# Kernel tuning notes

Hardware: AMD Instinct MI355X
Metric: run time of the kernel (lower is better)

## Reference

```python
import jax, jax.numpy as jnp
import numpy as np

TEMPERATURE = 2.0 / 3.0
LIMIT_A = -0.1
LIMIT_B = 1.1

N_NODES = 50000
N_CLUSTERS = 64
N_RELATIONS = 8
N_EDGES = 1000000


def setup_inputs() -> dict:
    key = jax.random.key(0)
    ks = jax.random.split(key, 6)
    xavier = float(np.sqrt(6.0 / (N_CLUSTERS + N_CLUSTERS)))
    return {
        "assignments": jax.random.normal(ks[0], (N_NODES, N_CLUSTERS), jnp.float32),
        "inter_cluster_logits": jax.random.uniform(ks[1], (N_RELATIONS, N_CLUSTERS, N_CLUSTERS), jnp.float32, -xavier, xavier),
        "log_alpha": jnp.zeros((N_RELATIONS, N_CLUSTERS, N_CLUSTERS), jnp.float32),
        "absent_bias": jnp.zeros((N_RELATIONS,), jnp.float32),
        "edge_index": jax.random.randint(ks[2], (2, N_EDGES), 0, N_NODES, jnp.int32),
        "edge_type": jax.random.randint(ks[3], (N_EDGES,), 0, N_RELATIONS, jnp.int32),
        "neg_edge_index": jax.random.randint(ks[4], (2, N_EDGES), 0, N_NODES, jnp.int32),
        "neg_edge_type": jax.random.randint(ks[5], (N_EDGES,), 0, N_RELATIONS, jnp.int32),
    }


def _edge_logits(assignments, weights, absent_bias, edge_index, edge_type):
    # src, dst: [E, C] gathers (irregular access)
    src = assignments[edge_index[0]]
    dst = assignments[edge_index[1]]
    n_rel = weights.shape[0]
    # torch.bmm(W[et], dst[:, :, None]) == dst @ W[et].T ; compute per relation
    # (fixed small relation loop; avoids materializing [E, C, C]) then select.
    logits_all = jnp.stack(
        [jnp.sum(src * (dst @ weights[r].T), axis=-1) for r in range(n_rel)],
        axis=-1,
    )  # [E, R]
    logits = jnp.take_along_axis(logits_all, edge_type[:, None], axis=1)[:, 0]
    return logits + absent_bias[edge_type]


def reference(assignments, inter_cluster_logits, log_alpha, absent_bias,
              edge_index, edge_type, neg_edge_index, neg_edge_type):
    # Hard-concrete gate, eval mode: z = clamp(sigmoid(log_alpha)*(b-a)+a, 0, 1)
    gate = jnp.clip(jax.nn.sigmoid(log_alpha) * (LIMIT_B - LIMIT_A) + LIMIT_A, 0.0, 1.0)
    weights = jax.nn.sigmoid(inter_cluster_logits) * gate  # [R, C, C]

    pos_logits = _edge_logits(assignments, weights, absent_bias, edge_index, edge_type)
    neg_logits = _edge_logits(assignments, weights, absent_bias, neg_edge_index, neg_edge_type)

    # BCE-with-logits: target=1 -> softplus(-x); target=0 -> softplus(x)
    pos_loss = jnp.mean(jax.nn.softplus(-pos_logits))
    neg_loss = jnp.mean(jax.nn.softplus(neg_logits))
    return pos_loss + neg_loss
```

## Files before the change

kernel.cpp:

```cpp
#include <hip/hip_runtime.h>
#include <hip/hip_bf16.h>
#include <math.h>

#define E_EDGES 1000000
#define N_NODES 50000
#define N_C     64
#define N_REL   8
#define CHB     2048
#define CAP     384
#define NBLK    489
#define BT      512
#define SENT    0xFFFFFFFFu

typedef __attribute__((ext_vector_type(4))) float floatx4;
typedef __attribute__((ext_vector_type(2))) float floatx2;

static __device__ __forceinline__ unsigned pk4_fp8(float a, float b, float c, float d) {
    unsigned w = 0;
    w = __builtin_amdgcn_cvt_pk_fp8_f32(a, b, w, false);
    w = __builtin_amdgcn_cvt_pk_fp8_f32(c, d, w, true);
    return w;
}

static __device__ __forceinline__ long long pack64(unsigned lo, unsigned hi) {
    uint2 u; u.x = lo; u.y = hi;
    return __builtin_bit_cast(long long, u);
}

__global__ __launch_bounds__(256) void prep_kernel(
    const float* __restrict__ assign,
    const float* __restrict__ icl,
    const float* __restrict__ la,
    unsigned char* __restrict__ Wp8,
    unsigned char* __restrict__ AS8,
    float* __restrict__ out)
{
    int tid = blockIdx.x * blockDim.x + threadIdx.x;
    int nth = gridDim.x * blockDim.x;
    if (tid == 0) out[0] = 0.0f;

    for (int idx = tid; idx < N_REL * N_C * 16; idx += nth) {
        int row = idx >> 4, dq = idx & 15;
        int q = dq >> 2, c = (dq >> 1) & 1, jh = dq & 1;
        int k0 = (2 * c + jh) * 16 + 4 * q;
        float wv[4];
        #pragma unroll
        for (int b = 0; b < 4; ++b) {
            int srci = (row << 6) + k0 + b;
            float w = 1.0f / (1.0f + __expf(-icl[srci]));
            float g = 1.0f / (1.0f + __expf(-la[srci])) * 1.2f - 0.1f;
            g = fminf(fmaxf(g, 0.0f), 1.0f);
            wv[b] = w * g;
        }
        ((unsigned*)Wp8)[idx] = pk4_fp8(wv[0], wv[1], wv[2], wv[3]);
    }

    for (int n = tid; n < N_NODES; n += nth) {
        const float4* a4 = (const float4*)(assign + (size_t)n * N_C);
        unsigned w[16];
        #pragma unroll
        for (int i = 0; i < 16; ++i) {
            float4 v = a4[i];
            w[i] = pk4_fp8(v.x, v.y, v.z, v.w);
        }
        uint4* as = (uint4*)(AS8 + (size_t)n * N_C);
        #pragma unroll
        for (int q = 0; q < 4; ++q) {
            uint4 o;
            o.x = w[0 * 4 + q];
            o.y = w[1 * 4 + q];
            o.z = w[2 * 4 + q];
            o.w = w[3 * 4 + q];
            as[q] = o;
        }
    }
}

__global__ __launch_bounds__(BT, 8) void edge_kernel(
    const unsigned char* __restrict__ AS8,
    const unsigned char* __restrict__ Wp8,
    const float* __restrict__ absent_bias,
    const int* __restrict__ ei, const int* __restrict__ et,
    const int* __restrict__ nei, const int* __restrict__ net,
    float* __restrict__ out)
{
    __shared__ unsigned list[N_REL * CAP];
    __shared__ unsigned cnt[N_REL];
    __shared__ float red[8];
    if (threadIdx.x < N_REL) cnt[threadIdx.x] = 0u;
    __syncthreads();

    int blk = blockIdx.x;
    bool isneg = blk >= NBLK;
    int lb = isneg ? blk - NBLK : blk;
    const int* Es = isneg ? nei : ei;
    const int* Et = isneg ? net : et;
    float sign = isneg ? 1.0f : -1.0f;
    int base = lb * CHB;
    int elim = min(base + CHB, E_EDGES);

    for (int e = base + threadIdx.x; e < elim; e += BT) {
        int s = Es[e];
        int d = Es[E_EDGES + e];
        int r = Et[e];
        unsigned rank = atomicAdd(&cnt[r], 1u);
        if (rank < CAP) list[r * CAP + rank] = (unsigned)s | ((unsigned)d << 16);
    }
    __syncthreads();

    if (threadIdx.x < N_REL * 16) {
        int r = threadIdx.x >> 4;
        int i = threadIdx.x & 15;
        int n = min((int)cnt[r], CAP);
        int padded = ((n + 15) >> 4) << 4;
        int slot = n + i;
        if (slot < padded) list[r * CAP + slot] = SENT;
    }
    __syncthreads();

    int lane = threadIdx.x & 63;
    int wid  = threadIdx.x >> 6;
    int n16  = lane & 15;
    int quad = lane >> 4;
    float loss = 0.0f;

    int G0 = (min((int)cnt[0], CAP) + 15) >> 4;
    int G1 = (min((int)cnt[1], CAP) + 15) >> 4;
    int G2 = (min((int)cnt[2], CAP) + 15) >> 4;
    int G3 = (min((int)cnt[3], CAP) + 15) >> 4;
    int G4 = (min((int)cnt[4], CAP) + 15) >> 4;
    int G5 = (min((int)cnt[5], CAP) + 15) >> 4;
    int G6 = (min((int)cnt[6], CAP) + 15) >> 4;
    int G7 = (min((int)cnt[7], CAP) + 15) >> 4;
    int go1 = G0;
    int go2 = go1 + G1;
    int go3 = go2 + G2;
    int go4 = go3 + G3;
    int go5 = go4 + G4;
    int go6 = go5 + G5;
    int go7 = go6 + G6;
    int tg  = go7 + G7;

    #define LOCATE(ITEM, R, GOF)                                   \
        do {                                                       \
            R = 0; GOF = 0;                                        \
            if ((ITEM) >= go1) { R = 1; GOF = go1; }               \
            if ((ITEM) >= go2) { R = 2; GOF = go2; }               \
            if ((ITEM) >= go3) { R = 3; GOF = go3; }               \
            if ((ITEM) >= go4) { R = 4; GOF = go4; }               \
            if ((ITEM) >= go5) { R = 5; GOF = go5; }               \
            if ((ITEM) >= go6) { R = 6; GOF = go6; }               \
            if ((ITEM) >= go7) { R = 7; GOF = go7; }               \
        } while (0)

    #define FETCH(ITEM, R, V, SREG, DREG)                                    \
        do {                                                                 \
            int gof_;                                                        \
            LOCATE(ITEM, R, gof_);                                           \
            unsigned rec_ = list[R * CAP + ((ITEM) - gof_) * 16 + n16];      \
            V = rec_ != SENT;                                                \
            unsigned sm_ = V ? (rec_ & 0xFFFFu) : 0u;                        \
            unsigned dm_ = V ? (rec_ >> 16) : 0u;                            \
            SREG = *(const uint4*)(AS8 + ((size_t)sm_ << 6) + quad * 16);    \
            DREG = *(const uint4*)(AS8 + ((size_t)dm_ << 6) + quad * 16);    \
        } while (0)

    int start = (wid * tg) >> 3;
    int end   = ((wid + 1) * tg) >> 3;

    int rC = 0;
    bool vC = false;
    uint4 SC = {0, 0, 0, 0}, DC = {0, 0, 0, 0};
    uint4 wfm[4];
    float bias = 0.0f;

    if (start < end) {
        FETCH(start, rC, vC, SC, DC);
        #pragma unroll
        for (int mt = 0; mt < 4; ++mt)
            wfm[mt] = *(const uint4*)(Wp8 + ((rC * 64 + mt * 16 + n16) << 6) + quad * 16);
        bias = absent_bias[rC];
    }

    for (int it = start; it < end; ++it) {
        int rN = rC;
        bool vN = false;
        uint4 SN = {0, 0, 0, 0}, DN = {0, 0, 0, 0};
        if (it + 1 < end) {
            FETCH(it + 1, rN, vN, SN, DN);
        }

        long long bD0 = pack64(DC.x, DC.y);
        long long bD1 = pack64(DC.z, DC.w);
        floatx4 ac[4];
        #pragma unroll
        for (int mt = 0; mt < 4; ++mt) {
            floatx4 z = {0.0f, 0.0f, 0.0f, 0.0f};
            z = __builtin_amdgcn_mfma_f32_16x16x32_fp8_fp8(
                    pack64(wfm[mt].x, wfm[mt].y), bD0, z, 0, 0, 0);
            ac[mt] = __builtin_amdgcn_mfma_f32_16x16x32_fp8_fp8(
                    pack64(wfm[mt].z, wfm[mt].w), bD1, z, 0, 0, 0);
        }
        unsigned sw[4] = {SC.x, SC.y, SC.z, SC.w};
        float d0 = 0.0f, d1 = 0.0f;
        #pragma unroll
        for (int mt = 0; mt < 4; mt += 2) {
            floatx2 lo0 = __builtin_amdgcn_cvt_pk_f32_fp8((int)sw[mt], false);
            floatx2 hi0 = __builtin_amdgcn_cvt_pk_f32_fp8((int)sw[mt], true);
            floatx2 lo1 = __builtin_amdgcn_cvt_pk_f32_fp8((int)sw[mt + 1], false);
            floatx2 hi1 = __builtin_amdgcn_cvt_pk_f32_fp8((int)sw[mt + 1], true);
            d0 = fmaf(lo0.x, ac[mt][0], d0);
            d1 = fmaf(lo1.x, ac[mt + 1][0], d1);
            d0 = fmaf(lo0.y, ac[mt][1], d0);
            d1 = fmaf(lo1.y, ac[mt + 1][1], d1);
            d0 = fmaf(hi0.x, ac[mt][2], d0);
            d1 = fmaf(hi1.x, ac[mt + 1][2], d1);
            d0 = fmaf(hi0.y, ac[mt][3], d0);
            d1 = fmaf(hi1.y, ac[mt + 1][3], d1);
        }
        float dot = d0 + d1;
        dot += __shfl_xor(dot, 16);
        dot += __shfl_xor(dot, 32);
        if (quad == 0 && vC) {
            float x = sign * (dot + bias);
            loss += fmaxf(x, 0.0f) + __logf(1.0f + __expf(-fabsf(x)));
        }

        if (rN != rC) {
            #pragma unroll
            for (int mt = 0; mt < 4; ++mt)
                wfm[mt] = *(const uint4*)(Wp8 + ((rN * 64 + mt * 16 + n16) << 6) + quad * 16);
            bias = absent_bias[rN];
            rC = rN;
        }
        vC = vN; SC = SN; DC = DN;
    }

    loss += __shfl_xor(loss, 1);
    loss += __shfl_xor(loss, 2);
    loss += __shfl_xor(loss, 4);
    loss += __shfl_xor(loss, 8);
    loss += __shfl_xor(loss, 16);
    loss += __shfl_xor(loss, 32);
    if (lane == 0) red[wid] = loss;
    __syncthreads();
    if (threadIdx.x == 0) {
        float t = red[0] + red[1] + red[2] + red[3]
                + red[4] + red[5] + red[6] + red[7];
        atomicAdd(out, t * (1.0f / (float)E_EDGES));
    }
}

extern "C" void kernel_launch(void* const* d_in, const int* in_sizes, int n_in,
                              void* d_out, int out_size, void* d_ws, size_t ws_size,
                              hipStream_t stream) {
    const float* assign = (const float*)d_in[0];
    const float* icl    = (const float*)d_in[1];
    const float* la     = (const float*)d_in[2];
    const float* ab     = (const float*)d_in[3];
    const int*   ei     = (const int*)d_in[4];
    const int*   et     = (const int*)d_in[5];
    const int*   nei    = (const int*)d_in[6];
    const int*   net    = (const int*)d_in[7];
    float* out = (float*)d_out;

    char* basep = (char*)d_ws;
    unsigned char* Wp8 = (unsigned char*)basep;
    unsigned char* AS8 = (unsigned char*)(basep + 65536);

    prep_kernel<<<256, 256, 0, stream>>>(assign, icl, la, Wp8, AS8, out);
    edge_kernel<<<2 * NBLK, BT, 0, stream>>>(AS8, Wp8, ab, ei, et, nei, net, out);
}
```

Before: 133.7 us.

## Deepen gather prefetch to two items ahead and interleave MFMA with reduction

```diff
diff --git a/kernel.cpp b/kernel.cpp
--- a/kernel.cpp
+++ b/kernel.cpp
@@ -6,9 +6,9 @@
 #define N_NODES 50000
 #define N_C     64
 #define N_REL   8
-#define CHB     2048
+#define CHB     1954
 #define CAP     384
-#define NBLK    489
+#define NBLK    512
 #define BT      512
 #define SENT    0xFFFFFFFFu
 
@@ -168,72 +168,79 @@
     int start = (wid * tg) >> 3;
     int end   = ((wid + 1) * tg) >> 3;
 
-    int rC = 0;
-    bool vC = false;
-    uint4 SC = {0, 0, 0, 0}, DC = {0, 0, 0, 0};
+    int r0 = 0, r1 = 0;
+    bool v0 = false, v1 = false;
+    uint4 S0 = {0,0,0,0}, D0 = {0,0,0,0};
+    uint4 S1 = {0,0,0,0}, D1 = {0,0,0,0};
     uint4 wfm[4];
     float bias = 0.0f;
+    const floatx4 zero4 = {0.0f, 0.0f, 0.0f, 0.0f};
 
     if (start < end) {
-        FETCH(start, rC, vC, SC, DC);
+        FETCH(start, r0, v0, S0, D0);
         #pragma unroll
         for (int mt = 0; mt < 4; ++mt)
-            wfm[mt] = *(const uint4*)(Wp8 + ((rC * 64 + mt * 16 + n16) << 6) + quad * 16);
-        bias = absent_bias[rC];
+            wfm[mt] = *(const uint4*)(Wp8 + ((r0 * 64 + mt * 16 + n16) << 6) + quad * 16);
+        bias = absent_bias[r0];
+        r1 = r0;
+        if (start + 1 < end) {
+            FETCH(start + 1, r1, v1, S1, D1);
+        }
     }
 
     for (int it = start; it < end; ++it) {
-        int rN = rC;
-        bool vN = false;
-        uint4 SN = {0, 0, 0, 0}, DN = {0, 0, 0, 0};
-        if (it + 1 < end) {
-            FETCH(it + 1, rN, vN, SN, DN);
-        }
-
-        long long bD0 = pack64(DC.x, DC.y);
-        long long bD1 = pack64(DC.z, DC.w);
-        floatx4 ac[4];
-        #pragma unroll
-        for (int mt = 0; mt < 4; ++mt) {
-            floatx4 z = {0.0f, 0.0f, 0.0f, 0.0f};
-            z = __builtin_amdgcn_mfma_f32_16x16x32_fp8_fp8(
-                    pack64(wfm[mt].x, wfm[mt].y), bD0, z, 0, 0, 0);
-            ac[mt] = __builtin_amdgcn_mfma_f32_16x16x32_fp8_fp8(
-                    pack64(wfm[mt].z, wfm[mt].w), bD1, z, 0, 0, 0);
-        }
-        unsigned sw[4] = {SC.x, SC.y, SC.z, SC.w};
+        int r2 = r1;
+        bool v2 = false;
+        uint4 S2 = {0,0,0,0}, D2 = {0,0,0,0};
+        if (it + 2 < end) {
+            FETCH(it + 2, r2, v2, S2, D2);
+        }
+
+        long long bD0 = pack64(D0.x, D0.y);
+        long long bD1 = pack64(D0.z, D0.w);
+        unsigned sw[4] = {S0.x, S0.y, S0.z, S0.w};
         float d0 = 0.0f, d1 = 0.0f;
         #pragma unroll
-        for (int mt = 0; mt < 4; mt += 2) {
-            floatx2 lo0 = __builtin_amdgcn_cvt_pk_f32_fp8((int)sw[mt], false);
-            floatx2 hi0 = __builtin_amdgcn_cvt_pk_f32_fp8((int)sw[mt], true);
-            floatx2 lo1 = __builtin_amdgcn_cvt_pk_f32_fp8((int)sw[mt + 1], false);
-            floatx2 hi1 = __builtin_amdgcn_cvt_pk_f32_fp8((int)sw[mt + 1], true);
-            d0 = fmaf(lo0.x, ac[mt][0], d0);
-            d1 = fmaf(lo1.x, ac[mt + 1][0], d1);
-            d0 = fmaf(lo0.y, ac[mt][1], d0);
-            d1 = fmaf(lo1.y, ac[mt + 1][1], d1);
-            d0 = fmaf(hi0.x, ac[mt][2], d0);
-            d1 = fmaf(hi1.x, ac[mt + 1][2], d1);
-            d0 = fmaf(hi0.y, ac[mt][3], d0);
-            d1 = fmaf(hi1.y, ac[mt + 1][3], d1);
+        for (int gidx = 0; gidx < 2; ++gidx) {
+            const int ma = 2 * gidx, mb = 2 * gidx + 1;
+            floatx4 p0 = zero4, p1 = zero4;
+            p0 = __builtin_amdgcn_mfma_f32_16x16x32_fp8_fp8(
+                    pack64(wfm[ma].x, wfm[ma].y), bD0, p0, 0, 0, 0);
+            p1 = __builtin_amdgcn_mfma_f32_16x16x32_fp8_fp8(
+                    pack64(wfm[mb].x, wfm[mb].y), bD0, p1, 0, 0, 0);
+            p0 = __builtin_amdgcn_mfma_f32_16x16x32_fp8_fp8(
+                    pack64(wfm[ma].z, wfm[ma].w), bD1, p0, 0, 0, 0);
+            p1 = __builtin_amdgcn_mfma_f32_16x16x32_fp8_fp8(
+                    pack64(wfm[mb].z, wfm[mb].w), bD1, p1, 0, 0, 0);
+            floatx2 lo0 = __builtin_amdgcn_cvt_pk_f32_fp8((int)sw[ma], false);
+            floatx2 hi0 = __builtin_amdgcn_cvt_pk_f32_fp8((int)sw[ma], true);
+            floatx2 lo1 = __builtin_amdgcn_cvt_pk_f32_fp8((int)sw[mb], false);
+            floatx2 hi1 = __builtin_amdgcn_cvt_pk_f32_fp8((int)sw[mb], true);
+            d0 = fmaf(lo0.x, p0[0], d0);
+            d1 = fmaf(lo1.x, p1[0], d1);
+            d0 = fmaf(lo0.y, p0[1], d0);
+            d1 = fmaf(lo1.y, p1[1], d1);
+            d0 = fmaf(hi0.x, p0[2], d0);
+            d1 = fmaf(hi1.x, p1[2], d1);
+            d0 = fmaf(hi0.y, p0[3], d0);
+            d1 = fmaf(hi1.y, p1[3], d1);
         }
         float dot = d0 + d1;
         dot += __shfl_xor(dot, 16);
         dot += __shfl_xor(dot, 32);
-        if (quad == 0 && vC) {
+        if (quad == 0 && v0) {
             float x = sign * (dot + bias);
             loss += fmaxf(x, 0.0f) + __logf(1.0f + __expf(-fabsf(x)));
         }
 
-        if (rN != rC) {
+        if (r1 != r0) {
             #pragma unroll
             for (int mt = 0; mt < 4; ++mt)
-                wfm[mt] = *(const uint4*)(Wp8 + ((rN * 64 + mt * 16 + n16) << 6) + quad * 16);
-            bias = absent_bias[rN];
-            rC = rN;
-        }
-        vC = vN; SC = SN; DC = DN;
+                wfm[mt] = *(const uint4*)(Wp8 + ((r1 * 64 + mt * 16 + n16) << 6) + quad * 16);
+            bias = absent_bias[r1];
+        }
+        r0 = r1; v0 = v1; S0 = S1; D0 = D1;
+        r1 = r2; v1 = v2; S1 = S2; D1 = D2;
     }
 
     loss += __shfl_xor(loss, 1);
```

New measurement: 190.5 us. 42.5% more time.
